# Kernel optimization log

Hardware: AMD Instinct MI355X
Metric: run time of the kernel (lower is better)

Reference implementation:

```python
import jax, jax.numpy as jnp
import numpy as np

GROUPS = 16
EPS = 1e-6


def conv1x1(x, w, b):
    # x: (B,C,N,K), w: (O,C), b: (O,)
    return jnp.einsum('oc,bcnk->bonk', w, x) + b[None, :, None, None]


def group_norm(x, gamma, beta):
    # GroupNorm(16, C, eps=1e-6, affine=True) over (C/g, N, K) per sample
    B, C, N, K = x.shape
    xg = x.reshape(B, GROUPS, C // GROUPS, N, K)
    mu = xg.mean(axis=(2, 3, 4), keepdims=True)
    var = xg.var(axis=(2, 3, 4), keepdims=True)
    xn = ((xg - mu) * jax.lax.rsqrt(var + EPS)).reshape(B, C, N, K)
    return xn * gamma[None, :, None, None] + beta[None, :, None, None]


def _gather_nbrs(x, idx):
    # x: (B,C,N), idx: (B,N,K) -> (B,C,N,K)
    return jax.vmap(lambda xb, ib: xb[:, ib])(x, idx)


def lse(coords_t, feats, idx, dist, w, b, g, bt):
    # LocalSpatialEncoding: coords_t (B,3,N), feats (B,C,N,1)
    nbr_coords = _gather_nbrs(coords_t, idx)                       # (B,3,N,K)
    ctr_coords = jnp.broadcast_to(coords_t[..., None], nbr_coords.shape)
    concat = jnp.concatenate(
        [ctr_coords, nbr_coords, ctr_coords - nbr_coords, dist[:, None]], axis=1)  # (B,10,N,K)
    enc = jax.nn.relu(group_norm(conv1x1(concat, w, b), g, bt))    # (B,C,N,K)
    nbr_feats = _gather_nbrs(feats[..., 0], idx)                   # (B,C,N,K)
    return jnp.concatenate([enc, nbr_feats], axis=1)               # (B,2C,N,K)


def attentive_pool(x, w, b, g, bt):
    # mean over K, then SharedMLP with GN+ReLU -> (B,O,N,1)
    m = x.mean(axis=-1, keepdims=True)
    return jax.nn.relu(group_norm(conv1x1(m, w, b), g, bt))


def setup_inputs() -> dict:
    B, N, K, D_IN, D_OUT = 2, 32768, 16, 72, 64
    H = D_OUT // 2  # 32
    key = jax.random.key(0)
    ks = jax.random.split(key, 24)

    def w(k, o, i):
        return jax.random.normal(k, (o, i), jnp.float32) * (1.0 / np.sqrt(i))

    inp = {
        'coords': jax.random.normal(ks[0], (B, N, 3), jnp.float32),
        'features': jax.random.normal(ks[1], (B, D_IN, N, 1), jnp.float32),
        'idx': jax.random.randint(ks[2], (B, N, K), 0, N, jnp.int32),
        'dist': jax.random.uniform(ks[3], (B, N, K), jnp.float32),
        # mlp1: d_in -> d_out//2, LeakyReLU(0.2)
        'w_mlp1': w(ks[4], H, D_IN), 'b_mlp1': jnp.zeros((H,), jnp.float32),
        # lse1 mlp: 10 -> H, GN+ReLU
        'w_lse1': w(ks[5], H, 10), 'b_lse1': jnp.zeros((H,), jnp.float32),
        'g_lse1': jnp.ones((H,), jnp.float32), 'bt_lse1': jnp.zeros((H,), jnp.float32),
        # pool1: d_out -> H, GN+ReLU
        'w_pool1': w(ks[6], H, D_OUT), 'b_pool1': jnp.zeros((H,), jnp.float32),
        'g_pool1': jnp.ones((H,), jnp.float32), 'bt_pool1': jnp.zeros((H,), jnp.float32),
        # lse2 mlp: 10 -> H
        'w_lse2': w(ks[7], H, 10), 'b_lse2': jnp.zeros((H,), jnp.float32),
        'g_lse2': jnp.ones((H,), jnp.float32), 'bt_lse2': jnp.zeros((H,), jnp.float32),
        # pool2: d_out -> d_out
        'w_pool2': w(ks[8], D_OUT, D_OUT), 'b_pool2': jnp.zeros((D_OUT,), jnp.float32),
        'g_pool2': jnp.ones((D_OUT,), jnp.float32), 'bt_pool2': jnp.zeros((D_OUT,), jnp.float32),
        # mlp2: d_out -> 2*d_out (no bn, no act)
        'w_mlp2': w(ks[9], 2 * D_OUT, D_OUT), 'b_mlp2': jnp.zeros((2 * D_OUT,), jnp.float32),
        # shortcut: d_in -> 2*d_out, GN, no act
        'w_sc': w(ks[10], 2 * D_OUT, D_IN), 'b_sc': jnp.zeros((2 * D_OUT,), jnp.float32),
        'g_sc': jnp.ones((2 * D_OUT,), jnp.float32), 'bt_sc': jnp.zeros((2 * D_OUT,), jnp.float32),
    }
    return inp


def reference(coords, features, idx, dist,
              w_mlp1, b_mlp1,
              w_lse1, b_lse1, g_lse1, bt_lse1,
              w_pool1, b_pool1, g_pool1, bt_pool1,
              w_lse2, b_lse2, g_lse2, bt_lse2,
              w_pool2, b_pool2, g_pool2, bt_pool2,
              w_mlp2, b_mlp2,
              w_sc, b_sc, g_sc, bt_sc):
    coords_t = coords.transpose(0, 2, 1)                        # (B,3,N)
    x = jax.nn.leaky_relu(conv1x1(features, w_mlp1, b_mlp1), 0.2)   # (B,32,N,1)
    x = lse(coords_t, x, idx, dist, w_lse1, b_lse1, g_lse1, bt_lse1)  # (B,64,N,K)
    x = attentive_pool(x, w_pool1, b_pool1, g_pool1, bt_pool1)        # (B,32,N,1)
    x = lse(coords_t, x, idx, dist, w_lse2, b_lse2, g_lse2, bt_lse2)  # (B,64,N,K)
    x = attentive_pool(x, w_pool2, b_pool2, g_pool2, bt_pool2)        # (B,64,N,1)
    main = conv1x1(x, w_mlp2, b_mlp2)                                 # (B,128,N,1)
    sc = group_norm(conv1x1(features, w_sc, b_sc), g_sc, bt_sc)       # (B,128,N,1)
    return jax.nn.leaky_relu(main + sc, 0.01)
```

## Files before the change

### kernel.cpp

```cpp
#include <hip/hip_runtime.h>

#define NN 32768
#define GEPS 1e-6f

__device__ __forceinline__ float wredsum(float v){
  v += __shfl_xor(v, 32); v += __shfl_xor(v, 16); v += __shfl_xor(v, 8);
  v += __shfl_xor(v, 4);  v += __shfl_xor(v, 2);  v += __shfl_xor(v, 1);
  return v;
}
__device__ __forceinline__ float eredsum(float v){
  v += __shfl_xor(v, 8); v += __shfl_xor(v, 16); v += __shfl_xor(v, 32);
  return v;
}
__device__ __forceinline__ float ecomb(float v){
  v += __shfl_xor(v, 1); v += __shfl_xor(v, 2); v += __shfl_xor(v, 4);
  return v;
}

__global__ void __launch_bounds__(256) f0_prep(
    const float* __restrict__ w_mlp1, const float* __restrict__ b_mlp1,
    const float* __restrict__ w_sc,   const float* __restrict__ b_sc,
    const float* __restrict__ w_pool1,const float* __restrict__ w_pool2,
    float* __restrict__ WallT, float* __restrict__ ball,
    float* __restrict__ wp1T,  float* __restrict__ wp2T)
{
  const int t0 = blockIdx.x*256 + threadIdx.x;
  const int stride = gridDim.x*256;
  for (int u=t0; u<72*160; u+=stride){
    int i = u/160, o = u - i*160;
    WallT[u] = (o < 128) ? w_sc[o*72+i] : w_mlp1[(o-128)*72+i];
  }
  for (int u=t0; u<160; u+=stride)
    ball[u] = (u < 128) ? b_sc[u] : b_mlp1[u-128];
  for (int u=t0; u<64*32; u+=stride){ int c=u>>5, o=u&31; wp1T[u] = w_pool1[o*64+c]; }
  for (int u=t0; u<64*64; u+=stride){ int c=u>>6, o=u&63; wp2T[u] = w_pool2[o*64+c]; }
}

__global__ void __launch_bounds__(256,2) k0_mlp1_scstats(
    const float* __restrict__ feat, const float* __restrict__ WallT,
    const float* __restrict__ ball,
    float* __restrict__ X1, float* __restrict__ scS, float* __restrict__ scQ)
{
  __shared__ float xl[72][128];
  __shared__ float wl[72*32];
  __shared__ float ssl[128], sql[128];
  const int tid = threadIdx.x, lane = tid & 63;
  const int wid = __builtin_amdgcn_readfirstlane(tid >> 6);
  const int b   = __builtin_amdgcn_readfirstlane((int)blockIdx.x >> 8);
  const int n0  = ((int)blockIdx.x & 255) << 7;
  const int p0  = lane*2;

  for (int u=tid; u<72*128; u+=256){
    int c = u>>7, j = u&127;
    xl[c][j] = feat[(size_t)(b*72+c)*NN + n0 + j];
  }

#pragma unroll 1
  for (int pass=0; pass<5; ++pass){
    __syncthreads();
    for (int u=tid; u<2304; u+=256){
      int i = u>>5, c = u&31;
      wl[u] = WallT[i*160 + pass*32 + c];
    }
    __syncthreads();

    const int oc = pass*32 + wid*8;
    float a0[8], a1[8];
#pragma unroll
    for (int q=0;q<8;q++){ float bv = ball[oc+q]; a0[q]=bv; a1[q]=bv; }

    const float* wbase = wl + wid*8;
#pragma unroll
    for (int i=0;i<72;i++){
      const float2 x2 = *(const float2*)&xl[i][p0];
      const float4 w0 = *(const float4*)(wbase + i*32);
      const float4 w1 = *(const float4*)(wbase + i*32 + 4);
      a0[0]=fmaf(w0.x,x2.x,a0[0]); a1[0]=fmaf(w0.x,x2.y,a1[0]);
      a0[1]=fmaf(w0.y,x2.x,a0[1]); a1[1]=fmaf(w0.y,x2.y,a1[1]);
      a0[2]=fmaf(w0.z,x2.x,a0[2]); a1[2]=fmaf(w0.z,x2.y,a1[2]);
      a0[3]=fmaf(w0.w,x2.x,a0[3]); a1[3]=fmaf(w0.w,x2.y,a1[3]);
      a0[4]=fmaf(w1.x,x2.x,a0[4]); a1[4]=fmaf(w1.x,x2.y,a1[4]);
      a0[5]=fmaf(w1.y,x2.x,a0[5]); a1[5]=fmaf(w1.y,x2.y,a1[5]);
      a0[6]=fmaf(w1.z,x2.x,a0[6]); a1[6]=fmaf(w1.z,x2.y,a1[6]);
      a0[7]=fmaf(w1.w,x2.x,a0[7]); a1[7]=fmaf(w1.w,x2.y,a1[7]);
    }

    if (pass < 4){
#pragma unroll
      for (int q=0;q<8;q++){
        float s  = wredsum(a0[q]+a1[q]);
        float s2 = wredsum(a0[q]*a0[q] + a1[q]*a1[q]);
        if (lane==0){ ssl[oc+q] = s; sql[oc+q] = s2; }
      }
    } else {
      __syncthreads();
      float* xst = &xl[0][0];
#pragma unroll
      for (int q=0;q<8;q++){
        float v0 = a0[q], v1 = a1[q];
        v0 = v0 > 0.f ? v0 : 0.2f*v0;
        v1 = v1 > 0.f ? v1 : 0.2f*v1;
        float2 t; t.x=v0; t.y=v1;
        *(float2*)&xst[(wid*8+q)*130 + p0] = t;
      }
      __syncthreads();
      float* xb = X1 + ((size_t)b*NN + n0)*32;
#pragma unroll
      for (int r=0;r<4;r++){
        int u = tid + r*256;
        int p = u>>3, c0 = (u&7)*4;
        float4 o;
        o.x = xst[(c0+0)*130+p]; o.y = xst[(c0+1)*130+p];
        o.z = xst[(c0+2)*130+p]; o.w = xst[(c0+3)*130+p];
        *(float4*)(xb + (size_t)p*32 + c0) = o;
      }
    }
  }

  if (tid < 128){
    atomicAdd(&scS[b*128+tid], ssl[tid]);
    atomicAdd(&scQ[b*128+tid], sql[tid]);
  }
}

__global__ void __launch_bounds__(256) k1_vmom(
    const float* __restrict__ coords, const int* __restrict__ idx,
    const float* __restrict__ dist, float* __restrict__ vm)
{
  __shared__ float red[4*65];
  const int tid = threadIdx.x, lane = tid & 63, wid = tid >> 6;
  const int gn = blockIdx.x*256 + tid;
  const int pt = gn >> 2, h = gn & 3;
  const int b = pt >> 15, n = pt & (NN-1);
  const size_t pb = (size_t)b*NN + n;
  const float c0 = coords[pb*3+0], c1 = coords[pb*3+1], c2 = coords[pb*3+2];

  int ja[4]; float da[4];
  {
    int4 j4 = *(const int4*)(idx + pb*16 + h*4);
    float4 d4 = *(const float4*)(dist + pb*16 + h*4);
    ja[0]=j4.x; ja[1]=j4.y; ja[2]=j4.z; ja[3]=j4.w;
    da[0]=d4.x; da[1]=d4.y; da[2]=d4.z; da[3]=d4.w;
  }

  float aS[10], aM[55];
#pragma unroll
  for (int i=0;i<10;i++) aS[i]=0.f;
#pragma unroll
  for (int i=0;i<55;i++) aM[i]=0.f;

#pragma unroll
  for (int k=0;k<4;k++){
    const float* nb = coords + ((size_t)b*NN + ja[k])*3;
    const float n0v=nb[0], n1v=nb[1], n2v=nb[2];
    const float v[10] = {c0,c1,c2,n0v,n1v,n2v,c0-n0v,c1-n1v,c2-n2v,da[k]};
#pragma unroll
    for (int i=0;i<10;i++){
      aS[i] += v[i];
#pragma unroll
      for (int j=i;j<10;j++)
        aM[i*10 - (i*(i-1))/2 + (j-i)] += v[i]*v[j];
    }
  }

#pragma unroll
  for (int i=0;i<10;i++){ float s = wredsum(aS[i]); if (lane==0) red[wid*65+i] = s; }
#pragma unroll
  for (int i=0;i<55;i++){ float s = wredsum(aM[i]); if (lane==0) red[wid*65+10+i] = s; }
  __syncthreads();
  if (tid < 65){
    float s = red[tid] + red[65+tid] + red[130+tid] + red[195+tid];
    const int bb = blockIdx.x >> 9;
    atomicAdd(&vm[bb*65+tid], s);
  }
}

__global__ void f1_fold(
    const float* __restrict__ w_lse1, const float* __restrict__ b_lse1,
    const float* __restrict__ g_lse1, const float* __restrict__ bt_lse1,
    const float* __restrict__ w_lse2, const float* __restrict__ b_lse2,
    const float* __restrict__ g_lse2, const float* __restrict__ bt_lse2,
    const float* __restrict__ vm,
    float* __restrict__ w1p, float* __restrict__ w2p)
{
  const int tid = threadIdx.x;
  const int half = tid >> 6;
  const int u = tid & 63, b = u >> 5, c = u & 31;
  const float* W  = half ? w_lse2  : w_lse1;
  const float* Bv = half ? b_lse2  : b_lse1;
  const float* G  = half ? g_lse2  : g_lse1;
  const float* Bt = half ? bt_lse2 : bt_lse1;
  float wr[10];
#pragma unroll
  for (int i=0;i<10;i++) wr[i] = W[c*10+i];
  const float* S = vm + b*65;
  const float* M = vm + b*65 + 10;
  float P = 0.f;
#pragma unroll
  for (int i=0;i<10;i++) P = fmaf(wr[i], S[i], P);
  float Q = 0.f;
#pragma unroll
  for (int i=0;i<10;i++){
#pragma unroll
    for (int j=i;j<10;j++){
      float m = M[i*10 - (i*(i-1))/2 + (j-i)];
      float t = wr[i]*wr[j]*m;
      Q += (i==j) ? t : 2.f*t;
    }
  }
  const float invNK = 1.f/((float)NN*16.f);
  const float bc = Bv[c];
  float mean = P*invNK + bc;
  float ey2  = (Q + 2.f*bc*P)*invNK + bc*bc;
  float mu = 0.5f*(mean + __shfl_xor(mean,1));
  float e2 = 0.5f*(ey2  + __shfl_xor(ey2, 1));
  float var = e2 - mu*mu;
  float rstd = rsqrtf(var + GEPS);
  float a = G[c]*rstd, d = Bt[c] - mu*a;
  float* out = (half ? w2p : w1p) + (b*32+c)*12;
#pragma unroll
  for (int i=0;i<10;i++) out[i] = wr[i]*a;
  out[10] = bc*a + d;
  out[11] = 0.f;
}

__global__ void __launch_bounds__(256,8) k2_lse1_pool1(
    const float* __restrict__ coords, const int* __restrict__ idx,
    const float* __restrict__ dist, const float* __restrict__ X1,
    const float* __restrict__ w1p, const float* __restrict__ wp1T,
    const float* __restrict__ b_pool1,
    float* __restrict__ Y1, float* __restrict__ p1S, float* __restrict__ p1Q)
{
  __shared__ float mfl[32*66];
  __shared__ float sl[32], ql[32];
  const int tid = threadIdx.x, lane = tid & 63;
  const int e = tid & 7;
  const int pl = tid >> 3;
  if (tid < 32){ sl[tid]=0.f; ql[tid]=0.f; }
  __syncthreads();
  const int b = __builtin_amdgcn_readfirstlane((int)blockIdx.x & 1);
  const int n = (((int)blockIdx.x >> 1) << 5) + pl;
  const size_t pb = (size_t)b*NN + n;
  float* mf = &mfl[pl*66];
  const float s16 = 0.0625f;

  {
    int ja[16];
    const int4* ip = (const int4*)(idx + pb*16);
#pragma unroll
    for (int k4=0;k4<4;k4++){
      int4 j4 = ip[k4];
      ja[k4*4+0]=j4.x; ja[k4*4+1]=j4.y; ja[k4*4+2]=j4.z; ja[k4*4+3]=j4.w;
    }
    float af0=0.f, af1=0.f, af2=0.f, af3=0.f;
    const float* xb = X1 + (size_t)b*NN*32 + e*4;
#pragma unroll 4
    for (int k=0;k<16;k++){
      float4 g = *(const float4*)(xb + (size_t)ja[k]*32);
      af0+=g.x; af1+=g.y; af2+=g.z; af3+=g.w;
    }
    mf[32+e*4+0]=af0*s16; mf[32+e*4+1]=af1*s16;
    mf[32+e*4+2]=af2*s16; mf[32+e*4+3]=af3*s16;
  }

  {
    int2 j2 = *(const int2*)(idx + pb*16 + e*2);
    float2 d2 = *(const float2*)(dist + pb*16 + e*2);
    const float* nb0 = coords + ((size_t)b*NN + j2.x)*3;
    const float* nb1 = coords + ((size_t)b*NN + j2.y)*3;
    const float nx0=nb0[0], ny0=nb0[1], nz0=nb0[2];
    const float nx1=nb1[0], ny1=nb1[1], nz1=nb1[2];
    const float c0=coords[pb*3], c1=coords[pb*3+1], c2=coords[pb*3+2];
    const float* wrow = w1p + (size_t)(b*32)*12;
#pragma unroll 1
    for (int cc=0;cc<4;cc++){
      float ptc[8];
#pragma unroll
      for (int q=0;q<8;q++){
        const float4* r4 = (const float4*)(wrow + (cc*8+q)*12);
        float4 ra=r4[0], rb=r4[1], rc=r4[2];
        const float t0=ra.x+rb.z, t1=ra.y+rb.w, t2=ra.z+rc.x;
        const float u0=ra.w-rb.z, u1=rb.x-rb.w, u2=rb.y-rc.x;
        const float wd=rc.y;
        float cb = rc.z;
        cb = fmaf(t0,c0,cb); cb = fmaf(t1,c1,cb); cb = fmaf(t2,c2,cb);
        float s0 = cb, s1 = cb;
        s0 = fmaf(u0,nx0,s0); s0 = fmaf(u1,ny0,s0); s0 = fmaf(u2,nz0,s0);
        s0 = fmaf(wd,d2.x,s0);
        s1 = fmaf(u0,nx1,s1); s1 = fmaf(u1,ny1,s1); s1 = fmaf(u2,nz1,s1);
        s1 = fmaf(wd,d2.y,s1);
        ptc[q] = fmaxf(s0,0.f) + fmaxf(s1,0.f);
      }
#pragma unroll
      for (int q=0;q<8;q++) ptc[q] = ecomb(ptc[q]);
      if ((e>>1)==cc){
        float v0 = (e&1) ? ptc[4] : ptc[0];
        float v1 = (e&1) ? ptc[5] : ptc[1];
        float v2 = (e&1) ? ptc[6] : ptc[2];
        float v3 = (e&1) ? ptc[7] : ptc[3];
        mf[e*4+0]=v0*s16; mf[e*4+1]=v1*s16;
        mf[e*4+2]=v2*s16; mf[e*4+3]=v3*s16;
      }
    }
  }
  __syncthreads();

  const int o0 = e*4;
  float yac[4];
  {
    const float4 b0 = *(const float4*)(b_pool1 + o0);
    yac[0]=b0.x; yac[1]=b0.y; yac[2]=b0.z; yac[3]=b0.w;
  }
#pragma unroll 4
  for (int c=0;c<64;c++){
    const float mc = mf[c];
    const float4 w0 = *(const float4*)(wp1T + c*32 + o0);
    yac[0]=fmaf(w0.x,mc,yac[0]); yac[1]=fmaf(w0.y,mc,yac[1]);
    yac[2]=fmaf(w0.z,mc,yac[2]); yac[3]=fmaf(w0.w,mc,yac[3]);
  }
  {
    float4 r0; r0.x=yac[0]; r0.y=yac[1]; r0.z=yac[2]; r0.w=yac[3];
    *(float4*)(Y1 + pb*32 + o0) = r0;
  }
#pragma unroll
  for (int q=0;q<4;q++){
    float s  = eredsum(yac[q]);
    float s2 = eredsum(yac[q]*yac[q]);
    if (lane < 8){ atomicAdd(&sl[o0+q], s); atomicAdd(&ql[o0+q], s2); }
  }
  __syncthreads();
  if (tid<32){ atomicAdd(&p1S[b*32+tid], sl[tid]); atomicAdd(&p1Q[b*32+tid], ql[tid]); }
}

__global__ void __launch_bounds__(256) f2_apply_pool1(
    float* __restrict__ Y1, const float* __restrict__ p1S, const float* __restrict__ p1Q,
    const float* __restrict__ g, const float* __restrict__ bt)
{
  __shared__ float al[32], dl[32];
  const int tid = threadIdx.x;
  const int b = blockIdx.x >> 10;
  if (tid < 32){
    float s = p1S[b*32+tid], q = p1Q[b*32+tid];
    s += __shfl_xor(s,1); q += __shfl_xor(q,1);
    const float inv = 1.f/(2.f*(float)NN);
    float mu = s*inv, e2 = q*inv, var = e2-mu*mu;
    float rstd = rsqrtf(var + GEPS);
    float a = g[tid]*rstd;
    al[tid] = a; dl[tid] = bt[tid] - mu*a;
  }
  __syncthreads();
  const size_t e4 = (size_t)blockIdx.x*256 + tid;
  float4* Y = (float4*)Y1;
  float4 v = Y[e4];
  const int c0 = ((int)(e4 & 7))*4;
  v.x = fmaxf(fmaf(v.x, al[c0+0], dl[c0+0]), 0.f);
  v.y = fmaxf(fmaf(v.y, al[c0+1], dl[c0+1]), 0.f);
  v.z = fmaxf(fmaf(v.z, al[c0+2], dl[c0+2]), 0.f);
  v.w = fmaxf(fmaf(v.w, al[c0+3], dl[c0+3]), 0.f);
  Y[e4] = v;
}

__global__ void __launch_bounds__(256,8) k4_lse2_pool2(
    const float* __restrict__ coords, const int* __restrict__ idx,
    const float* __restrict__ dist, const float* __restrict__ Y1,
    const float* __restrict__ w2p, const float* __restrict__ wp2T,
    const float* __restrict__ b_pool2,
    float* __restrict__ Y2T, float* __restrict__ p2S, float* __restrict__ p2Q)
{
  __shared__ float mfl[32*66];
  __shared__ float sl[64], ql[64];
  const int tid = threadIdx.x, lane = tid & 63;
  const int e = tid & 7;
  const int pl = tid >> 3;
  if (tid < 64){ sl[tid]=0.f; ql[tid]=0.f; }
  __syncthreads();
  const int b = __builtin_amdgcn_readfirstlane((int)blockIdx.x & 1);
  const int n0g = (((int)blockIdx.x >> 1) << 5);
  const int n = n0g + pl;
  const size_t pb = (size_t)b*NN + n;
  float* mf = &mfl[pl*66];
  const float s16 = 0.0625f;

  {
    int ja[16];
    const int4* ip = (const int4*)(idx + pb*16);
#pragma unroll
    for (int k4=0;k4<4;k4++){
      int4 j4 = ip[k4];
      ja[k4*4+0]=j4.x; ja[k4*4+1]=j4.y; ja[k4*4+2]=j4.z; ja[k4*4+3]=j4.w;
    }
    float af0=0.f, af1=0.f, af2=0.f, af3=0.f;
    const float* yb = Y1 + (size_t)b*NN*32 + e*4;
#pragma unroll 4
    for (int k=0;k<16;k++){
      float4 g = *(const float4*)(yb + (size_t)ja[k]*32);
      af0+=g.x; af1+=g.y; af2+=g.z; af3+=g.w;
    }
    mf[32+e*4+0]=af0*s16; mf[32+e*4+1]=af1*s16;
    mf[32+e*4+2]=af2*s16; mf[32+e*4+3]=af3*s16;
  }

  {
    int2 j2 = *(const int2*)(idx + pb*16 + e*2);
    float2 d2 = *(const float2*)(dist + pb*16 + e*2);
    const float* nb0 = coords + ((size_t)b*NN + j2.x)*3;
    const float* nb1 = coords + ((size_t)b*NN + j2.y)*3;
    const float nx0=nb0[0], ny0=nb0[1], nz0=nb0[2];
    const float nx1=nb1[0], ny1=nb1[1], nz1=nb1[2];
    const float c0=coords[pb*3], c1=coords[pb*3+1], c2=coords[pb*3+2];
    const float* wrow = w2p + (size_t)(b*32)*12;
#pragma unroll 1
    for (int cc=0;cc<4;cc++){
      float ptc[8];
#pragma unroll
      for (int q=0;q<8;q++){
        const float4* r4 = (const float4*)(wrow + (cc*8+q)*12);
        float4 ra=r4[0], rb=r4[1], rc=r4[2];
        const float t0=ra.x+rb.z, t1=ra.y+rb.w, t2=ra.z+rc.x;
        const float u0=ra.w-rb.z, u1=rb.x-rb.w, u2=rb.y-rc.x;
        const float wd=rc.y;
        float cb = rc.z;
        cb = fmaf(t0,c0,cb); cb = fmaf(t1,c1,cb); cb = fmaf(t2,c2,cb);
        float s0 = cb, s1 = cb;
        s0 = fmaf(u0,nx0,s0); s0 = fmaf(u1,ny0,s0); s0 = fmaf(u2,nz0,s0);
        s0 = fmaf(wd,d2.x,s0);
        s1 = fmaf(u0,nx1,s1); s1 = fmaf(u1,ny1,s1); s1 = fmaf(u2,nz1,s1);
        s1 = fmaf(wd,d2.y,s1);
        ptc[q] = fmaxf(s0,0.f) + fmaxf(s1,0.f);
      }
#pragma unroll
      for (int q=0;q<8;q++) ptc[q] = ecomb(ptc[q]);
      if ((e>>1)==cc){
        float v0 = (e&1) ? ptc[4] : ptc[0];
        float v1 = (e&1) ? ptc[5] : ptc[1];
        float v2 = (e&1) ? ptc[6] : ptc[2];
        float v3 = (e&1) ? ptc[7] : ptc[3];
        mf[e*4+0]=v0*s16; mf[e*4+1]=v1*s16;
        mf[e*4+2]=v2*s16; mf[e*4+3]=v3*s16;
      }
    }
  }
  __syncthreads();

  const int o0 = e*8;
  float yac[8];
  {
    const float4 b0 = *(const float4*)(b_pool2 + o0);
    const float4 b1 = *(const float4*)(b_pool2 + o0 + 4);
    yac[0]=b0.x; yac[1]=b0.y; yac[2]=b0.z; yac[3]=b0.w;
    yac[4]=b1.x; yac[5]=b1.y; yac[6]=b1.z; yac[7]=b1.w;
  }
#pragma unroll 4
  for (int c=0;c<64;c++){
    const float mc = mf[c];
    const float4 w0 = *(const float4*)(wp2T + c*64 + o0);
    const float4 w1 = *(const float4*)(wp2T + c*64 + o0 + 4);
    yac[0]=fmaf(w0.x,mc,yac[0]); yac[1]=fmaf(w0.y,mc,yac[1]);
    yac[2]=fmaf(w0.z,mc,yac[2]); yac[3]=fmaf(w0.w,mc,yac[3]);
    yac[4]=fmaf(w1.x,mc,yac[4]); yac[5]=fmaf(w1.y,mc,yac[5]);
    yac[6]=fmaf(w1.z,mc,yac[6]); yac[7]=fmaf(w1.w,mc,yac[7]);
  }
#pragma unroll
  for (int q=0;q<8;q++){
    float s  = eredsum(yac[q]);
    float s2 = eredsum(yac[q]*yac[q]);
    if (lane < 8){ atomicAdd(&sl[o0+q], s); atomicAdd(&ql[o0+q], s2); }
  }
  __syncthreads();
  float* ldsT = &mfl[0];
#pragma unroll
  for (int o=0;o<8;o++) ldsT[(o0+o)*33 + pl] = yac[o];
  __syncthreads();
#pragma unroll
  for (int r=0;r<8;r++){
    int u = tid + r*256;
    int ch = u >> 5, p = u & 31;
    Y2T[((size_t)(b*64+ch))*NN + n0g + p] = ldsT[ch*33 + p];
  }
  if (tid<64){ atomicAdd(&p2S[b*64+tid], sl[tid]); atomicAdd(&p2Q[b*64+tid], ql[tid]); }
}

__global__ void f3a_affines(
    const float* __restrict__ scS, const float* __restrict__ scQ,
    const float* __restrict__ g_sc, const float* __restrict__ bt_sc,
    const float* __restrict__ b_sc, const float* __restrict__ b_mlp2,
    const float* __restrict__ p2S, const float* __restrict__ p2Q,
    const float* __restrict__ g_p2, const float* __restrict__ bt_p2,
    float* __restrict__ ascT, float* __restrict__ cstF,
    float* __restrict__ a2F, float* __restrict__ d2F)
{
  const int tid = threadIdx.x;
  if (tid < 256){
    const int b = tid >> 7, c = tid & 127;
    float s = scS[b*128+c], q = scQ[b*128+c];
    s += __shfl_xor(s,1); q += __shfl_xor(q,1);
    s += __shfl_xor(s,2); q += __shfl_xor(q,2);
    s += __shfl_xor(s,4); q += __shfl_xor(q,4);
    const float inv = 1.f/(8.f*(float)NN);
    float mu = s*inv, e2 = q*inv, var = e2-mu*mu;
    float rstd = rsqrtf(var + GEPS);
    float a = g_sc[c]*rstd;
    ascT[tid] = a;
    cstF[tid] = b_mlp2[c] + a*b_sc[c] + (bt_sc[c] - mu*a);
  } else {
    const int t = tid - 256;
    const int b = t >> 6, c = t & 63;
    float s = p2S[b*64+c], q = p2Q[b*64+c];
    s += __shfl_xor(s,1); q += __shfl_xor(q,1);
    s += __shfl_xor(s,2); q += __shfl_xor(q,2);
    const float inv = 1.f/(4.f*(float)NN);
    float mu = s*inv, e2 = q*inv, var = e2-mu*mu;
    float rstd = rsqrtf(var + GEPS);
    float a = g_p2[c]*rstd;
    a2F[t] = a; d2F[t] = bt_p2[c] - mu*a;
  }
}

__global__ void __launch_bounds__(256) f3b_wcomb(
    const float* __restrict__ w_mlp2, const float* __restrict__ w_sc,
    const float* __restrict__ ascT, float* __restrict__ Wcomb)
{
  const int t0 = blockIdx.x*256 + threadIdx.x;
  const int stride = gridDim.x*256;
  for (int u=t0; u<2*136*128; u+=stride){
    int bb = u / 17408;
    int rr = u - bb*17408;
    int i = rr >> 7, o = rr & 127;
    Wcomb[u] = (i < 64) ? w_mlp2[o*64+i]
                        : w_sc[o*72 + (i-64)] * ascT[bb*128+o];
  }
}

__global__ void __launch_bounds__(256,3) k6_final(
    const float* __restrict__ feat, const float* __restrict__ Y2T,
    const float* __restrict__ Wcomb, const float* __restrict__ cstF,
    const float* __restrict__ a2F, const float* __restrict__ d2F,
    float* __restrict__ out)
{
  __shared__ float xl[136][64];
  __shared__ float wl[136*32];
  const int tid = threadIdx.x, lane = tid & 63;
  const int wid = __builtin_amdgcn_readfirstlane(tid >> 6);
  const int b   = __builtin_amdgcn_readfirstlane((int)blockIdx.x >> 9);
  const int n0  = ((int)blockIdx.x & 511) << 6;

  for (int u=tid; u<64*64; u+=256){
    int c = u>>6, j = u&63;
    float y = Y2T[(size_t)(b*64+c)*NN + n0 + j];
    xl[c][j] = fmaxf(fmaf(y, a2F[b*64+c], d2F[b*64+c]), 0.f);
  }
  for (int u=tid; u<72*64; u+=256){
    int c = u>>6, j = u&63;
    xl[64+c][j] = feat[(size_t)(b*72+c)*NN + n0 + j];
  }

  const float* Wb = Wcomb + b*17408;
#pragma unroll 1
  for (int pass=0; pass<4; ++pass){
    __syncthreads();
    for (int u=tid; u<4352; u+=256){
      int i = u>>5, c = u&31;
      wl[u] = Wb[i*128 + pass*32 + c];
    }
    __syncthreads();

    const int oc = pass*32 + wid*8;
    float acc[8];
#pragma unroll
    for (int q=0;q<8;q++) acc[q] = cstF[b*128+oc+q];

    const float* wbase = wl + wid*8;
#pragma unroll
    for (int i=0;i<136;i++){
      const float x = xl[i][lane];
      const float4 w0 = *(const float4*)(wbase + i*32);
      const float4 w1 = *(const float4*)(wbase + i*32 + 4);
      acc[0]=fmaf(w0.x,x,acc[0]); acc[1]=fmaf(w0.y,x,acc[1]);
      acc[2]=fmaf(w0.z,x,acc[2]); acc[3]=fmaf(w0.w,x,acc[3]);
      acc[4]=fmaf(w1.x,x,acc[4]); acc[5]=fmaf(w1.y,x,acc[5]);
      acc[6]=fmaf(w1.z,x,acc[6]); acc[7]=fmaf(w1.w,x,acc[7]);
    }
#pragma unroll
    for (int q=0;q<8;q++){
      float r = acc[q];
      out[((size_t)(b*128+oc+q))*NN + n0 + lane] = r > 0.f ? r : 0.01f*r;
    }
  }
}

extern "C" void kernel_launch(void* const* d_in, const int* in_sizes, int n_in,
                              void* d_out, int out_size, void* d_ws, size_t ws_size,
                              hipStream_t stream) {
  (void)in_sizes; (void)n_in; (void)out_size; (void)ws_size;
  const float* coords  = (const float*)d_in[0];
  const float* feats   = (const float*)d_in[1];
  const int*   idx     = (const int*)  d_in[2];
  const float* dist    = (const float*)d_in[3];
  const float* w_mlp1  = (const float*)d_in[4];
  const float* b_mlp1  = (const float*)d_in[5];
  const float* w_lse1  = (const float*)d_in[6];
  const float* b_lse1  = (const float*)d_in[7];
  const float* g_lse1  = (const float*)d_in[8];
  const float* bt_lse1 = (const float*)d_in[9];
  const float* w_pool1 = (const float*)d_in[10];
  const float* b_pool1 = (const float*)d_in[11];
  const float* g_pool1 = (const float*)d_in[12];
  const float* bt_pool1= (const float*)d_in[13];
  const float* w_lse2  = (const float*)d_in[14];
  const float* b_lse2  = (const float*)d_in[15];
  const float* g_lse2  = (const float*)d_in[16];
  const float* bt_lse2 = (const float*)d_in[17];
  const float* w_pool2 = (const float*)d_in[18];
  const float* b_pool2 = (const float*)d_in[19];
  const float* g_pool2 = (const float*)d_in[20];
  const float* bt_pool2= (const float*)d_in[21];
  const float* w_mlp2  = (const float*)d_in[22];
  const float* b_mlp2  = (const float*)d_in[23];
  const float* w_sc    = (const float*)d_in[24];
  const float* b_sc    = (const float*)d_in[25];
  const float* g_sc    = (const float*)d_in[26];
  const float* bt_sc   = (const float*)d_in[27];

  float* ws   = (float*)d_ws;
  float* scS  = ws;
  float* scQ  = ws + 256;
  float* vm   = ws + 512;
  float* p1S  = ws + 704;
  float* p1Q  = ws + 768;
  float* p2S  = ws + 832;
  float* p2Q  = ws + 960;
  float* w1p  = ws + 1280;
  float* w2p  = ws + 2048;
  float* wp1T = ws + 2816;
  float* wp2T = ws + 4864;
  float* ball = ws + 8960;
  float* cstF = ws + 9120;
  float* a2F  = ws + 9376;
  float* d2F  = ws + 9504;
  float* ascT = ws + 9632;
  float* WallT= ws + 9984;
  float* Wcomb= ws + 21504;
  float* X1   = ws + 57344;
  float* Y1   = X1 + (size_t)2*NN*32;
  float* Y2T  = Y1 + (size_t)2*NN*32;

  hipMemsetAsync(d_ws, 0, 1088*sizeof(float), stream);

  f0_prep<<<32,256,0,stream>>>(w_mlp1,b_mlp1,w_sc,b_sc,w_pool1,w_pool2,
                               WallT,ball,wp1T,wp2T);
  k0_mlp1_scstats<<<512,256,0,stream>>>(feats, WallT, ball, X1, scS, scQ);
  k1_vmom<<<1024,256,0,stream>>>(coords, idx, dist, vm);
  f1_fold<<<1,128,0,stream>>>(w_lse1,b_lse1,g_lse1,bt_lse1,
                              w_lse2,b_lse2,g_lse2,bt_lse2,
                              vm, w1p, w2p);
  k2_lse1_pool1<<<2048,256,0,stream>>>(coords, idx, dist, X1, w1p, wp1T, b_pool1,
                                       Y1, p1S, p1Q);
  f2_apply_pool1<<<2048,256,0,stream>>>(Y1, p1S, p1Q, g_pool1, bt_pool1);
  k4_lse2_pool2<<<2048,256,0,stream>>>(coords, idx, dist, Y1, w2p, wp2T, b_pool2,
                                       Y2T, p2S, p2Q);
  f3a_affines<<<1,384,0,stream>>>(scS,scQ,g_sc,bt_sc,b_sc,b_mlp2,
                                  p2S,p2Q,g_pool2,bt_pool2, ascT,cstF,a2F,d2F);
  f3b_wcomb<<<64,256,0,stream>>>(w_mlp2, w_sc, ascT, Wcomb);
  k6_final<<<1024,256,0,stream>>>(feats, Y2T, Wcomb, cstF, a2F, d2F, (float*)d_out);
}
```

Before: 265.1 us.

## Retile final GEMM kernel to 2 points x 16 channels per thread

Result: slower. 277.6 us (+4.7%).

```diff
diff --git a/kernel.cpp b/kernel.cpp
--- a/kernel.cpp
+++ b/kernel.cpp
@@ -537,53 +537,75 @@
     const float* __restrict__ a2F, const float* __restrict__ d2F,
     float* __restrict__ out)
 {
-  __shared__ float xl[136][64];
-  __shared__ float wl[136*32];
+  __shared__ float xl[68*128];
+  __shared__ float wl[68*64];
   const int tid = threadIdx.x, lane = tid & 63;
   const int wid = __builtin_amdgcn_readfirstlane(tid >> 6);
-  const int b   = __builtin_amdgcn_readfirstlane((int)blockIdx.x >> 9);
-  const int n0  = ((int)blockIdx.x & 511) << 6;
-
-  for (int u=tid; u<64*64; u+=256){
-    int c = u>>6, j = u&63;
-    float y = Y2T[(size_t)(b*64+c)*NN + n0 + j];
-    xl[c][j] = fmaxf(fmaf(y, a2F[b*64+c], d2F[b*64+c]), 0.f);
-  }
-  for (int u=tid; u<72*64; u+=256){
-    int c = u>>6, j = u&63;
-    xl[64+c][j] = feat[(size_t)(b*72+c)*NN + n0 + j];
-  }
-
-  const float* Wb = Wcomb + b*17408;
+  const int g   = __builtin_amdgcn_readfirstlane((int)blockIdx.x >> 9);
+  const int b   = __builtin_amdgcn_readfirstlane(((int)blockIdx.x >> 8) & 1);
+  const int n0  = ((int)blockIdx.x & 255) << 7;
+  const int p0  = lane*2;
+
+  float acc[2][2][8];
+#pragma unroll
+  for (int ps=0; ps<2; ps++){
+#pragma unroll
+    for (int q=0;q<8;q++){
+      float bv = cstF[b*128 + g*64 + ps*32 + wid*8 + q];
+      acc[ps][0][q]=bv; acc[ps][1][q]=bv;
+    }
+  }
+
+  const float* Wb = Wcomb + b*17408 + g*64;
 #pragma unroll 1
-  for (int pass=0; pass<4; ++pass){
+  for (int half=0; half<2; ++half){
     __syncthreads();
-    for (int u=tid; u<4352; u+=256){
-      int i = u>>5, c = u&31;
-      wl[u] = Wb[i*128 + pass*32 + c];
+    for (int u=tid; u<68*128; u+=256){
+      int row = u>>7, j = u&127;
+      int r = half*68 + row;
+      float v;
+      if (r < 64){
+        float y = Y2T[(size_t)(b*64+r)*NN + n0 + j];
+        v = fmaxf(fmaf(y, a2F[b*64+r], d2F[b*64+r]), 0.f);
+      } else {
+        v = feat[(size_t)(b*72 + (r-64))*NN + n0 + j];
+      }
+      xl[u] = v;
+    }
+    for (int u=tid; u<68*64; u+=256){
+      int i = u>>6, c = u&63;
+      wl[u] = Wb[(size_t)(half*68+i)*128 + c];
     }
     __syncthreads();
 
-    const int oc = pass*32 + wid*8;
-    float acc[8];
-#pragma unroll
-    for (int q=0;q<8;q++) acc[q] = cstF[b*128+oc+q];
-
     const float* wbase = wl + wid*8;
-#pragma unroll
-    for (int i=0;i<136;i++){
-      const float x = xl[i][lane];
-      const float4 w0 = *(const float4*)(wbase + i*32);
-      const float4 w1 = *(const float4*)(wbase + i*32 + 4);
-      acc[0]=fmaf(w0.x,x,acc[0]); acc[1]=fmaf(w0.y,x,acc[1]);
-      acc[2]=fmaf(w0.z,x,acc[2]); acc[3]=fmaf(w0.w,x,acc[3]);
-      acc[4]=fmaf(w1.x,x,acc[4]); acc[5]=fmaf(w1.y,x,acc[5]);
-      acc[6]=fmaf(w1.z,x,acc[6]); acc[7]=fmaf(w1.w,x,acc[7]);
-    }
+#pragma unroll 2
+    for (int i=0;i<68;i++){
+      const float2 x2 = *(const float2*)&xl[i*128 + p0];
+#pragma unroll
+      for (int ps=0; ps<2; ps++){
+        const float4 wA = *(const float4*)(wbase + i*64 + ps*32);
+        const float4 wB = *(const float4*)(wbase + i*64 + ps*32 + 4);
+        const float wv[8] = {wA.x,wA.y,wA.z,wA.w,wB.x,wB.y,wB.z,wB.w};
+#pragma unroll
+        for (int q=0;q<8;q++){
+          acc[ps][0][q] = fmaf(wv[q], x2.x, acc[ps][0][q]);
+          acc[ps][1][q] = fmaf(wv[q], x2.y, acc[ps][1][q]);
+        }
+      }
+    }
+  }
+
+#pragma unroll
+  for (int ps=0; ps<2; ps++){
 #pragma unroll
     for (int q=0;q<8;q++){
-      float r = acc[q];
-      out[((size_t)(b*128+oc+q))*NN + n0 + lane] = r > 0.f ? r : 0.01f*r;
+      const int ch = b*128 + g*64 + ps*32 + wid*8 + q;
+      float v0 = acc[ps][0][q], v1 = acc[ps][1][q];
+      float2 r;
+      r.x = v0 > 0.f ? v0 : 0.01f*v0;
+      r.y = v1 > 0.f ? v1 : 0.01f*v1;
+      *(float2*)(out + (size_t)ch*NN + n0 + p0) = r;
     }
   }
 }
```
